# Optimization experiments

Measured on AMD Instinct MI355X. Metric: run time of the kernel, lower is better.

## Reference

```python
import jax, jax.numpy as jnp
import numpy as np

PS = 2      # patch_size
TOPK = 3    # topk


def setup_inputs() -> dict:
    key = jax.random.key(0)
    x = jax.random.normal(key, (16, 128, 64, 64), dtype=jnp.float32)
    alpha = jnp.asarray(5.0, dtype=jnp.float32)
    return {"x": x, "alpha": alpha}


def reference(x, alpha):
    ps = PS
    b, c, h, w = x.shape
    nph, npw = h // ps, w // ps
    npatch = nph * npw
    pa = ps * ps
    # F.normalize(x, p=2, dim=-3): L2-normalize over channels
    nrm = jnp.sqrt(jnp.sum(x * x, axis=1, keepdims=True))
    x = x / jnp.maximum(nrm, 1e-12)
    # patchify: [b,c,h,w] -> [b,c,num_patches,patch_area]
    x = x.reshape(b * c * nph, ps, npw, ps)
    x = jnp.swapaxes(x, 1, 2).reshape(b, c, npatch, pa)
    diag = np.arange(ps) * (ps + 1)          # diagonal positions within a patch
    x = x[:, :, :, diag]                     # [b,c,npatch,ps]
    x = jnp.swapaxes(x, 1, 3)                # [b,ps,npatch,c]
    # per-diagonal-pixel patch correlation matrix
    corr = jnp.einsum('bpnc,bpmc->bpnm', x, x)           # [b,ps,np,np]
    avg = jnp.mean(corr, axis=1, keepdims=True)
    corr = jnp.concatenate([corr, avg], axis=1)          # [b,ps+1,np,np]
    # gaussian self-suppression mask (1 - gaussian centered at each patch)
    rat_s = 0.05
    sr, sc = nph * rat_s, npw * rat_s
    ind_r = jnp.arange(nph, dtype=jnp.float32).reshape(1, nph, 1)
    ind_c = jnp.arange(npw, dtype=jnp.float32).reshape(1, 1, npw)
    cr, cc = jnp.meshgrid(jnp.arange(nph, dtype=jnp.float32),
                          jnp.arange(npw, dtype=jnp.float32), indexing='ij')
    cent_r = cr.reshape(npatch, 1, 1)
    cent_c = cc.reshape(npatch, 1, 1)
    g = jnp.exp(-(ind_r - cent_r) ** 2 / (2.0 * sr * sr)) \
        * jnp.exp(-(ind_c - cent_c) ** 2 / (2.0 * sc * sc))   # [np,nph,npw]
    mask = (1.0 - g).reshape(1, 1, npatch, npatch)
    s = (corr * mask) * alpha
    # dual (row + column) softmax
    a = jax.nn.softmax(s, axis=-1) * jax.nn.softmax(s, axis=-2)  # [b,ps+1,np,np]
    # scatter: diagonal in-patch pixels get their own map, rest get the avg map
    src = np.full(pa, ps, dtype=np.int64)
    src[diag] = np.arange(ps)
    a = a[:, src]                              # [b,pa,np,np]
    # un-patchify attention back to [b, npatch, h, w]
    a = jnp.swapaxes(a, 1, 3)                  # [b,np,np,pa]
    a = a.reshape(b * npatch * nph, npw, ps, ps)
    a = jnp.swapaxes(a, 1, 2)
    a = a.reshape(b, npatch, h, w)
    # top-k over the patch (correlation-source) dim
    vals = jax.lax.top_k(jnp.moveaxis(a, 1, -1), TOPK)[0]  # [b,h,w,k]
    return jnp.moveaxis(vals, -1, 1)           # [b,k,h,w]
```

## Files before the change

### kernel.cpp

```cpp
#include <hip/hip_runtime.h>
#include <math.h>

#define NB 16
#define NCH 128
#define NH 64
#define NW 64
#define NP 1024

#define TN 32
#define TM 128
#define KC 32
#define KP 36
#define PK 40

#define NTILE 144

typedef __attribute__((ext_vector_type(8))) short short8v;
typedef __attribute__((ext_vector_type(4))) float f32x4;

__device__ __forceinline__ float med3(float a, float b, float c) {
  return __builtin_amdgcn_fmed3f(a, b, c);
}
__device__ __forceinline__ void top3_ins(float& t0, float& t1, float& t2, float a) {
  float n0 = fmaxf(t0, a);
  float n1 = med3(a, t0, t1);
  float n2 = med3(a, t1, t2);
  t0 = n0; t1 = n1; t2 = n2;
}
__device__ __forceinline__ float dot4(float4 a, float4 b) {
  return a.x * b.x + a.y * b.y + a.z * b.z + a.w * b.w;
}
__device__ __forceinline__ ushort f2bf(float f) {
  unsigned u = __float_as_uint(f);
  unsigned r = (u + 0x7FFFu + ((u >> 16) & 1u)) >> 16;
  return (ushort)r;
}
__device__ __forceinline__ float bf2f(ushort h) {
  return __uint_as_float(((unsigned)h) << 16);
}

__global__ __launch_bounds__(256) void prep_split(const float* __restrict__ x,
                                                  ushort* __restrict__ Vs,
                                                  float* __restrict__ rsum) {
  int blk = blockIdx.x;
  int t = threadIdx.x;
  int gid = blk * 256 + t;
  if (gid < NB * 3 * NP) rsum[gid] = 0.f;

  int b = blk >> 5;
  int c = (blk >> 4) & 1;
  int ng = blk & 15;
  int nl = t >> 2;
  int kq = t & 3;
  int n = ng * 64 + nl;
  int i = 2 * (n >> 5) + c;
  int j = 2 * (n & 31) + c;
  const float* xp = x + (size_t)b * NCH * NH * NW + i * NW + j;

  float v[32];
#pragma unroll
  for (int e = 0; e < 32; ++e)
    v[e] = xp[(size_t)(kq * 32 + e) * NH * NW];

  float ss = 0.f;
#pragma unroll
  for (int e = 0; e < 32; ++e) ss += v[e] * v[e];
  ss += __shfl_xor(ss, 1, 64);
  ss += __shfl_xor(ss, 2, 64);
  float r = 1.0f / fmaxf(sqrtf(ss), 1e-12f);

  size_t base = ((size_t)(b * 2 + c) * 3) * NP * NCH + (size_t)n * NCH + kq * 32;
  ushort* p1 = Vs + base;
  ushort* p2 = Vs + base + (size_t)NP * NCH;
  ushort* p3 = Vs + base + (size_t)2 * NP * NCH;
#pragma unroll
  for (int kg2 = 0; kg2 < 4; ++kg2) {
    ushort h1[8], h2[8], h3[8];
#pragma unroll
    for (int e = 0; e < 8; ++e) {
      float vv = v[kg2 * 8 + e] * r;
      ushort a = f2bf(vv);
      float r1 = vv - bf2f(a);
      ushort bq = f2bf(r1);
      float r2 = r1 - bf2f(bq);
      ushort cq = f2bf(r2);
      h1[e] = a; h2[e] = bq; h3[e] = cq;
    }
    *(float4*)(p1 + kg2 * 8) = *(float4*)h1;
    *(float4*)(p2 + kg2 * 8) = *(float4*)h2;
    *(float4*)(p3 + kg2 * 8) = *(float4*)h3;
  }
}

__global__ __launch_bounds__(256, 2) void gemm_mfma(
    const ushort* __restrict__ Vs, const float* __restrict__ alpha_p,
    float2* __restrict__ Sbuf, float* __restrict__ rsum) {
  __shared__ __align__(16) char smem[2 * 3 * 32 * PK * 2 + 2 * 3 * 128 * PK * 2];
  ushort (*A_s)[3][32][PK] = reinterpret_cast<ushort(*)[3][32][PK]>(smem);
  ushort (*B_s)[3][128][PK] =
      reinterpret_cast<ushort(*)[3][128][PK]>(smem + 2 * 3 * 32 * PK * 2);
  float2 (*Ts)[33] = reinterpret_cast<float2(*)[33]>(smem);

  const int b = blockIdx.y;
  int id = blockIdx.x;
  int g = 0;
  while (id >= 4 * (8 - g)) { id -= 4 * (8 - g); ++g; }
  const int ni = 4 * g + id / (8 - g);
  const int mj = g + id % (8 - g);
  const int n0 = ni * TN;
  const int m0 = mj * TM;

  const int t = threadIdx.x;
  const int lane = t & 63, wv = t >> 6;
  const int jc = lane & 15, kg = lane >> 4;
  const float alpha = *alpha_p;
  const ushort* Vsb = Vs + (size_t)b * 6 * NP * NCH;
  float* rs = rsum + (size_t)b * 3 * NP;

  f32x4 acc[2][2][2];
#pragma unroll
  for (int c = 0; c < 2; ++c)
#pragma unroll
    for (int i = 0; i < 2; ++i)
#pragma unroll
      for (int j = 0; j < 2; ++j) acc[c][i][j] = (f32x4){0.f, 0.f, 0.f, 0.f};

  for (int k0 = 0; k0 < NCH; k0 += KC) {
    __syncthreads();
#pragma unroll
    for (int q = 0; q < 3; ++q) {
      int flat = q * 256 + t;
      int p = flat >> 7;
      int rem = flat & 127;
      int row = rem >> 2, u = rem & 3;
      const ushort* src = Vsb + ((size_t)p * NP + n0 + row) * NCH + k0 + u * 8;
      *(float4*)&A_s[p / 3][p % 3][row][u * 8] = *(const float4*)src;
    }
#pragma unroll
    for (int q = 0; q < 12; ++q) {
      int flat = q * 256 + t;
      int p = flat >> 9;
      int rem = flat & 511;
      int row = rem >> 2, u = rem & 3;
      const ushort* src = Vsb + ((size_t)p * NP + m0 + row) * NCH + k0 + u * 8;
      *(float4*)&B_s[p / 3][p % 3][row][u * 8] = *(const float4*)src;
    }
    __syncthreads();

#pragma unroll
    for (int c = 0; c < 2; ++c) {
      short8v a1n0 = *(const short8v*)&A_s[c][0][jc][kg * 8];
      short8v a1n1 = *(const short8v*)&A_s[c][0][16 + jc][kg * 8];
      short8v a2n0 = *(const short8v*)&A_s[c][1][jc][kg * 8];
      short8v a2n1 = *(const short8v*)&A_s[c][1][16 + jc][kg * 8];
      short8v a3n0 = *(const short8v*)&A_s[c][2][jc][kg * 8];
      short8v a3n1 = *(const short8v*)&A_s[c][2][16 + jc][kg * 8];
      {
        short8v b0 = *(const short8v*)&B_s[c][0][wv * 32 + jc][kg * 8];
        short8v b1 = *(const short8v*)&B_s[c][0][wv * 32 + 16 + jc][kg * 8];
        acc[c][0][0] = __builtin_amdgcn_mfma_f32_16x16x32_bf16(a1n0, b0, acc[c][0][0], 0, 0, 0);
        acc[c][1][0] = __builtin_amdgcn_mfma_f32_16x16x32_bf16(a1n1, b0, acc[c][1][0], 0, 0, 0);
        acc[c][0][1] = __builtin_amdgcn_mfma_f32_16x16x32_bf16(a1n0, b1, acc[c][0][1], 0, 0, 0);
        acc[c][1][1] = __builtin_amdgcn_mfma_f32_16x16x32_bf16(a1n1, b1, acc[c][1][1], 0, 0, 0);
        acc[c][0][0] = __builtin_amdgcn_mfma_f32_16x16x32_bf16(a2n0, b0, acc[c][0][0], 0, 0, 0);
        acc[c][1][0] = __builtin_amdgcn_mfma_f32_16x16x32_bf16(a2n1, b0, acc[c][1][0], 0, 0, 0);
        acc[c][0][1] = __builtin_amdgcn_mfma_f32_16x16x32_bf16(a2n0, b1, acc[c][0][1], 0, 0, 0);
        acc[c][1][1] = __builtin_amdgcn_mfma_f32_16x16x32_bf16(a2n1, b1, acc[c][1][1], 0, 0, 0);
        acc[c][0][0] = __builtin_amdgcn_mfma_f32_16x16x32_bf16(a3n0, b0, acc[c][0][0], 0, 0, 0);
        acc[c][1][0] = __builtin_amdgcn_mfma_f32_16x16x32_bf16(a3n1, b0, acc[c][1][0], 0, 0, 0);
        acc[c][0][1] = __builtin_amdgcn_mfma_f32_16x16x32_bf16(a3n0, b1, acc[c][0][1], 0, 0, 0);
        acc[c][1][1] = __builtin_amdgcn_mfma_f32_16x16x32_bf16(a3n1, b1, acc[c][1][1], 0, 0, 0);
      }
      {
        short8v b0 = *(const short8v*)&B_s[c][1][wv * 32 + jc][kg * 8];
        short8v b1 = *(const short8v*)&B_s[c][1][wv * 32 + 16 + jc][kg * 8];
        acc[c][0][0] = __builtin_amdgcn_mfma_f32_16x16x32_bf16(a1n0, b0, acc[c][0][0], 0, 0, 0);
        acc[c][1][0] = __builtin_amdgcn_mfma_f32_16x16x32_bf16(a1n1, b0, acc[c][1][0], 0, 0, 0);
        acc[c][0][1] = __builtin_amdgcn_mfma_f32_16x16x32_bf16(a1n0, b1, acc[c][0][1], 0, 0, 0);
        acc[c][1][1] = __builtin_amdgcn_mfma_f32_16x16x32_bf16(a1n1, b1, acc[c][1][1], 0, 0, 0);
        acc[c][0][0] = __builtin_amdgcn_mfma_f32_16x16x32_bf16(a2n0, b0, acc[c][0][0], 0, 0, 0);
        acc[c][1][0] = __builtin_amdgcn_mfma_f32_16x16x32_bf16(a2n1, b0, acc[c][1][0], 0, 0, 0);
        acc[c][0][1] = __builtin_amdgcn_mfma_f32_16x16x32_bf16(a2n0, b1, acc[c][0][1], 0, 0, 0);
        acc[c][1][1] = __builtin_amdgcn_mfma_f32_16x16x32_bf16(a2n1, b1, acc[c][1][1], 0, 0, 0);
      }
      {
        short8v b0 = *(const short8v*)&B_s[c][2][wv * 32 + jc][kg * 8];
        short8v b1 = *(const short8v*)&B_s[c][2][wv * 32 + 16 + jc][kg * 8];
        acc[c][0][0] = __builtin_amdgcn_mfma_f32_16x16x32_bf16(a1n0, b0, acc[c][0][0], 0, 0, 0);
        acc[c][1][0] = __builtin_amdgcn_mfma_f32_16x16x32_bf16(a1n1, b0, acc[c][1][0], 0, 0, 0);
        acc[c][0][1] = __builtin_amdgcn_mfma_f32_16x16x32_bf16(a1n0, b1, acc[c][0][1], 0, 0, 0);
        acc[c][1][1] = __builtin_amdgcn_mfma_f32_16x16x32_bf16(a1n1, b1, acc[c][1][1], 0, 0, 0);
      }
    }
  }

  __syncthreads();
  float e[2][4][3];
#pragma unroll
  for (int ns = 0; ns < 2; ++ns)
#pragma unroll
    for (int r = 0; r < 4; ++r)
#pragma unroll
      for (int c = 0; c < 3; ++c) e[ns][r][c] = 0.f;

#pragma unroll
  for (int ns = 0; ns < 2; ++ns) {
#pragma unroll
    for (int r = 0; r < 4; ++r) {
      int nl = ns * 16 + kg * 4 + r;
      int n = n0 + nl;
      int nr = n >> 5, nc = n & 31;
      float2* rowp = Sbuf + ((size_t)b * NP + n) * NP;
#pragma unroll
      for (int ms = 0; ms < 2; ++ms) {
        int ml = wv * 32 + ms * 16 + jc;
        int m = m0 + ml;
        int dr = nr - (m >> 5);
        int dc = nc - (m & 31);
        float gss = __expf(-(float)(dr * dr + dc * dc) * 0.1953125f);
        float wgt = (1.0f - gss) * alpha;
        float2 sv = make_float2(acc[0][ns][ms][r] * wgt, acc[1][ns][ms][r] * wgt);
        Ts[ml][nl] = sv;
        if (m >= n) {
          rowp[m] = sv;
          e[ns][r][0] += __expf(sv.x);
          e[ns][r][1] += __expf(sv.y);
          e[ns][r][2] += __expf(0.5f * (sv.x + sv.y));
        }
      }
    }
  }
#pragma unroll
  for (int off = 1; off < 16; off <<= 1) {
#pragma unroll
    for (int ns = 0; ns < 2; ++ns)
#pragma unroll
      for (int r = 0; r < 4; ++r)
#pragma unroll
        for (int c = 0; c < 3; ++c)
          e[ns][r][c] += __shfl_xor(e[ns][r][c], off, 64);
  }
  if (jc == 0) {
#pragma unroll
    for (int ns = 0; ns < 2; ++ns)
#pragma unroll
      for (int r = 0; r < 4; ++r)
#pragma unroll
        for (int c = 0; c < 3; ++c)
          atomicAdd(&rs[(size_t)c * NP + (n0 + ns * 16 + kg * 4 + r)], e[ns][r][c]);
  }

  __syncthreads();
#pragma unroll
  for (int q = 0; q < 16; ++q) {
    int flat = q * 256 + t;
    int ml = flat >> 5;
    int r = flat & 31;
    int m = m0 + ml;
    int n = n0 + r;
    if (m > n) Sbuf[((size_t)b * NP + m) * NP + n] = Ts[ml][r];
  }
  {
    int ml = t >> 1;
    int rh = (t & 1) * 16;
    int m = m0 + ml;
    float e0 = 0.f, e1 = 0.f, e2 = 0.f;
#pragma unroll
    for (int rr = 0; rr < 16; ++rr) {
      int r = rh + rr;
      int n = n0 + r;
      float2 sv = Ts[ml][r];
      if (m > n) {
        e0 += __expf(sv.x);
        e1 += __expf(sv.y);
        e2 += __expf(0.5f * (sv.x + sv.y));
      }
    }
    e0 += __shfl_xor(e0, 1, 64);
    e1 += __shfl_xor(e1, 1, 64);
    e2 += __shfl_xor(e2, 1, 64);
    if ((t & 1) == 0) {
      atomicAdd(&rs[(size_t)0 * NP + m], e0);
      atomicAdd(&rs[(size_t)1 * NP + m], e1);
      atomicAdd(&rs[(size_t)2 * NP + m], e2);
    }
  }
}

__global__ __launch_bounds__(256) void recip_kernel(float* __restrict__ p, int nelem) {
  int i = blockIdx.x * 256 + threadIdx.x;
  if (i < nelem) p[i] = 1.0f / p[i];
}

__global__ __launch_bounds__(256, 4) void topk_kernel(
    const float2* __restrict__ Sbuf, const float* __restrict__ rinv,
    float* __restrict__ out) {
  const int n = blockIdx.x, b = blockIdx.y;
  const int t = threadIdx.x;
  const float* rb = rinv + (size_t)b * 3 * NP;
  float rin[3];
#pragma unroll
  for (int c = 0; c < 3; ++c) rin[c] = rb[c * NP + n];
  const float2* row = Sbuf + ((size_t)b * NP + n) * NP;

  float t0[3] = {0.f, 0.f, 0.f}, t1[3] = {0.f, 0.f, 0.f}, t2[3] = {0.f, 0.f, 0.f};
#pragma unroll
  for (int q = 0; q < 4; ++q) {
    int m = t + q * 256;
    float2 s01 = row[m];
    float s[3];
    s[0] = s01.x; s[1] = s01.y; s[2] = 0.5f * (s01.x + s01.y);
#pragma unroll
    for (int c = 0; c < 3; ++c) {
      float a = __expf(2.0f * s[c]) * rin[c] * rb[c * NP + m];
      top3_ins(t0[c], t1[c], t2[c], a);
    }
  }
#pragma unroll
  for (int off = 1; off < 64; off <<= 1) {
#pragma unroll
    for (int c = 0; c < 3; ++c) {
      float o0 = __shfl_xor(t0[c], off, 64);
      float o1 = __shfl_xor(t1[c], off, 64);
      float o2 = __shfl_xor(t2[c], off, 64);
      top3_ins(t0[c], t1[c], t2[c], o0);
      top3_ins(t0[c], t1[c], t2[c], o1);
      top3_ins(t0[c], t1[c], t2[c], o2);
    }
  }
  __shared__ float lds[4][9];
  if ((t & 63) == 0) {
    int w = t >> 6;
#pragma unroll
    for (int c = 0; c < 3; ++c) {
      lds[w][c * 3 + 0] = t0[c];
      lds[w][c * 3 + 1] = t1[c];
      lds[w][c * 3 + 2] = t2[c];
    }
  }
  __syncthreads();
  if (t == 0) {
#pragma unroll
    for (int w = 1; w < 4; ++w)
#pragma unroll
      for (int c = 0; c < 3; ++c) {
        top3_ins(t0[c], t1[c], t2[c], lds[w][c * 3 + 0]);
        top3_ins(t0[c], t1[c], t2[c], lds[w][c * 3 + 1]);
        top3_ins(t0[c], t1[c], t2[c], lds[w][c * 3 + 2]);
      }
    int pr = n >> 5, pc = n & 31;
#pragma unroll
    for (int c = 0; c < 3; ++c) {
      int ii0, jj0, ii1 = -1, jj1 = -1;
      if (c == 0)      { ii0 = 2 * pr;     jj0 = 2 * pc; }
      else if (c == 1) { ii0 = 2 * pr + 1; jj0 = 2 * pc + 1; }
      else             { ii0 = 2 * pr;     jj0 = 2 * pc + 1;
                         ii1 = 2 * pr + 1; jj1 = 2 * pc; }
      out[(((size_t)b * 3 + 0) * NH + ii0) * NW + jj0] = t0[c];
      out[(((size_t)b * 3 + 1) * NH + ii0) * NW + jj0] = t1[c];
      out[(((size_t)b * 3 + 2) * NH + ii0) * NW + jj0] = t2[c];
      if (ii1 >= 0) {
        out[(((size_t)b * 3 + 0) * NH + ii1) * NW + jj1] = t0[c];
        out[(((size_t)b * 3 + 1) * NH + ii1) * NW + jj1] = t1[c];
        out[(((size_t)b * 3 + 2) * NH + ii1) * NW + jj1] = t2[c];
      }
    }
  }
}

__global__ __launch_bounds__(256) void prep_kernel(const float* __restrict__ x,
                                                   float* __restrict__ V) {
  int blk = blockIdx.x;
  int t = threadIdx.x;
  int b = blk >> 3;
  int c = (blk >> 2) & 1;
  int n = (blk & 3) * 256 + t;
  int i = 2 * (n >> 5) + c;
  int j = 2 * (n & 31) + c;
  const float* xp = x + (size_t)b * NCH * NH * NW + i * NW + j;
  float ss = 0.f;
#pragma unroll 8
  for (int ch = 0; ch < NCH; ++ch) {
    float v = xp[(size_t)ch * NH * NW];
    ss += v * v;
  }
  float r = 1.0f / fmaxf(sqrtf(ss), 1e-12f);
  float* vp = V + (((size_t)b * 2 + c) * NP + n) * NCH;
#pragma unroll 8
  for (int ch = 0; ch < NCH; ++ch) {
    vp[ch] = xp[(size_t)ch * NH * NW] * r;
  }
}

template <int PASS>
__global__ __launch_bounds__(256, 2) void corr_kernel(
    const float* __restrict__ V, const float* __restrict__ alpha_p,
    float* __restrict__ rsum_g, float* __restrict__ out) {
  __shared__ __align__(16) float As[2][TN][KP];
  __shared__ __align__(16) float Bs[2][TM][KP];

  const int b = blockIdx.y;
  const int n0 = blockIdx.x * TN;
  const int t = threadIdx.x;
  const int tx = t & 31;
  const int ty = t >> 5;
  const float alpha = *alpha_p;
  const float* Vb = V + (size_t)b * 2 * NP * NCH;

  float sm[3][4];
  float t0[3][4], t1[3][4], t2[3][4];
  float rin[3][4];
#pragma unroll
  for (int c = 0; c < 3; ++c)
#pragma unroll
    for (int i = 0; i < 4; ++i) {
      sm[c][i] = 0.f;
      t0[c][i] = 0.f; t1[c][i] = 0.f; t2[c][i] = 0.f;
    }
  if (PASS == 2) {
#pragma unroll
    for (int c = 0; c < 3; ++c)
#pragma unroll
      for (int i = 0; i < 4; ++i) {
        int n = n0 + ty * 4 + i;
        rin[c][i] = 1.0f / rsum_g[((size_t)b * 3 + c) * NP + n];
      }
  }

  for (int mc = 0; mc < NP / TM; ++mc) {
    const int m0 = mc * TM;
    float acc[2][4][4];
#pragma unroll
    for (int c = 0; c < 2; ++c)
#pragma unroll
      for (int i = 0; i < 4; ++i)
#pragma unroll
        for (int j = 0; j < 4; ++j) acc[c][i][j] = 0.f;

    for (int k0 = 0; k0 < NCH; k0 += KC) {
      __syncthreads();
#pragma unroll
      for (int q = 0; q < 2; ++q) {
        int flat = q * 256 + t;
        int c = flat >> 8;
        int rem = flat & 255;
        int row = rem >> 3;
        int kgx = rem & 7;
        float4 v4 = *(const float4*)(Vb + ((size_t)c * NP + n0 + row) * NCH + k0 + kgx * 4);
        *(float4*)&As[c][row][kgx * 4] = v4;
      }
#pragma unroll
      for (int q = 0; q < 8; ++q) {
        int flat = q * 256 + t;
        int c = flat >> 10;
        int rem = flat & 1023;
        int row = rem >> 3;
        int kgx = rem & 7;
        float4 v4 = *(const float4*)(Vb + ((size_t)c * NP + m0 + row) * NCH + k0 + kgx * 4);
        *(float4*)&Bs[c][row][kgx * 4] = v4;
      }
      __syncthreads();

      for (int kgx = 0; kgx < KC; kgx += 4) {
        float4 a4[2][4], b4[2][4];
#pragma unroll
        for (int c = 0; c < 2; ++c)
#pragma unroll
          for (int i = 0; i < 4; ++i)
            a4[c][i] = *(const float4*)&As[c][ty * 4 + i][kgx];
#pragma unroll
        for (int c = 0; c < 2; ++c)
#pragma unroll
          for (int j = 0; j < 4; ++j)
            b4[c][j] = *(const float4*)&Bs[c][tx + 32 * j][kgx];
#pragma unroll
        for (int c = 0; c < 2; ++c)
#pragma unroll
          for (int i = 0; i < 4; ++i)
#pragma unroll
            for (int j = 0; j < 4; ++j)
              acc[c][i][j] += dot4(a4[c][i], b4[c][j]);
      }
    }

    float rim[3][4];
    if (PASS == 2) {
#pragma unroll
      for (int c = 0; c < 3; ++c)
#pragma unroll
        for (int j = 0; j < 4; ++j) {
          int m = m0 + tx + 32 * j;
          rim[c][j] = 1.0f / rsum_g[((size_t)b * 3 + c) * NP + m];
        }
    }
#pragma unroll
    for (int i = 0; i < 4; ++i) {
      int n = n0 + ty * 4 + i;
      int nr = n >> 5, nc = n & 31;
      float s[3][4];
#pragma unroll
      for (int j = 0; j < 4; ++j) {
        int m = m0 + tx + 32 * j;
        int dr = nr - (m >> 5);
        int dc = nc - (m & 31);
        float gq = __expf(-(float)(dr * dr + dc * dc) * 0.1953125f);
        float wgt = (1.0f - gq) * alpha;
        float s0v = acc[0][i][j] * wgt;
        float s1v = acc[1][i][j] * wgt;
        s[0][j] = s0v; s[1][j] = s1v; s[2][j] = 0.5f * (s0v + s1v);
      }
      if (PASS == 1) {
#pragma unroll
        for (int c = 0; c < 3; ++c) {
          sm[c][i] += __expf(s[c][0]) + __expf(s[c][1]) +
                      __expf(s[c][2]) + __expf(s[c][3]);
        }
      } else {
#pragma unroll
        for (int c = 0; c < 3; ++c) {
#pragma unroll
          for (int j = 0; j < 4; ++j) {
            float a = __expf(2.0f * s[c][j]) * rin[c][i] * rim[c][j];
            top3_ins(t0[c][i], t1[c][i], t2[c][i], a);
          }
        }
      }
    }
  }

  if (PASS == 1) {
#pragma unroll
    for (int off = 1; off < 32; off <<= 1) {
#pragma unroll
      for (int c = 0; c < 3; ++c)
#pragma unroll
        for (int i = 0; i < 4; ++i)
          sm[c][i] += __shfl_xor(sm[c][i], off, 64);
    }
    if (tx == 0) {
#pragma unroll
      for (int c = 0; c < 3; ++c)
#pragma unroll
        for (int i = 0; i < 4; ++i) {
          int n = n0 + ty * 4 + i;
          rsum_g[((size_t)b * 3 + c) * NP + n] = sm[c][i];
        }
    }
  } else {
#pragma unroll
    for (int off = 1; off < 32; off <<= 1) {
#pragma unroll
      for (int c = 0; c < 3; ++c)
#pragma unroll
        for (int i = 0; i < 4; ++i) {
          float o0 = __shfl_xor(t0[c][i], off, 64);
          float o1 = __shfl_xor(t1[c][i], off, 64);
          float o2 = __shfl_xor(t2[c][i], off, 64);
          top3_ins(t0[c][i], t1[c][i], t2[c][i], o0);
          top3_ins(t0[c][i], t1[c][i], t2[c][i], o1);
          top3_ins(t0[c][i], t1[c][i], t2[c][i], o2);
        }
    }
    if (tx == 0) {
#pragma unroll
      for (int c = 0; c < 3; ++c)
#pragma unroll
        for (int i = 0; i < 4; ++i) {
          int n = n0 + ty * 4 + i;
          int pr = n >> 5, pc = n & 31;
          float v0 = t0[c][i], v1 = t1[c][i], v2 = t2[c][i];
          int ii0, jj0, ii1 = -1, jj1 = -1;
          if (c == 0)      { ii0 = 2 * pr;     jj0 = 2 * pc; }
          else if (c == 1) { ii0 = 2 * pr + 1; jj0 = 2 * pc + 1; }
          else             { ii0 = 2 * pr;     jj0 = 2 * pc + 1;
                             ii1 = 2 * pr + 1; jj1 = 2 * pc; }
          out[(((size_t)b * 3 + 0) * NH + ii0) * NW + jj0] = v0;
          out[(((size_t)b * 3 + 1) * NH + ii0) * NW + jj0] = v1;
          out[(((size_t)b * 3 + 2) * NH + ii0) * NW + jj0] = v2;
          if (ii1 >= 0) {
            out[(((size_t)b * 3 + 0) * NH + ii1) * NW + jj1] = v0;
            out[(((size_t)b * 3 + 1) * NH + ii1) * NW + jj1] = v1;
            out[(((size_t)b * 3 + 2) * NH + ii1) * NW + jj1] = v2;
          }
        }
    }
  }
}

extern "C" void kernel_launch(void* const* d_in, const int* in_sizes, int n_in,
                              void* d_out, int out_size, void* d_ws, size_t ws_size,
                              hipStream_t stream) {
  const float* x = (const float*)d_in[0];
  const float* alpha = (const float*)d_in[1];
  float* out = (float*)d_out;

  const size_t nVsU = (size_t)NB * 6 * NP * NCH;
  const size_t nRs = (size_t)NB * 3 * NP;
  const size_t nS = (size_t)NB * NP * NP;

  ushort* Vs = (ushort*)d_ws;
  float* rsum = (float*)(Vs + nVsU);
  float2* Sbuf = (float2*)(rsum + nRs);

  const size_t need_bytes = nVsU * 2 + nRs * 4 + nS * 8;

  if (ws_size >= need_bytes) {
    prep_split<<<512, 256, 0, stream>>>(x, Vs, rsum);
    gemm_mfma<<<dim3(NTILE, NB), 256, 0, stream>>>(Vs, alpha, Sbuf, rsum);
    recip_kernel<<<(NB * 3 * NP + 255) / 256, 256, 0, stream>>>(rsum, NB * 3 * NP);
    topk_kernel<<<dim3(NP, NB), 256, 0, stream>>>(Sbuf, rsum, out);
  } else {
    float* V = (float*)d_ws;
    float* rsum_f = V + (size_t)NB * 2 * NP * NCH;
    prep_kernel<<<128, 256, 0, stream>>>(x, V);
    corr_kernel<1><<<dim3(NP / TN, NB), 256, 0, stream>>>(V, alpha, rsum_f, out);
    corr_kernel<2><<<dim3(NP / TN, NB), 256, 0, stream>>>(V, alpha, rsum_f, out);
  }
}
```

Measured before the change: 148.6 us.

## Recompute correlation tiles in top-k kernel instead of materializing score matrix

The full 1024x1024 score matrix per batch is no longer written to and read back from global memory. The first GEMM pass now only accumulates softmax row and column exp-sums, with the transposed column sums reduced in registers through shuffles instead of an LDS transpose. A new MFMA top-k kernel recomputes the split-bf16 correlation for a 16-row strip against all columns and applies the dual-softmax and top-3 selection on the fly. This removes a large HBM round trip in exchange for recomputing the full, non-symmetric GEMM and re-reading the B operand from cache once per 16-row strip.

```diff
diff --git a/kernel.cpp b/kernel.cpp
--- a/kernel.cpp
+++ b/kernel.cpp
@@ -92,14 +92,13 @@
   }
 }
 
-__global__ __launch_bounds__(256, 2) void gemm_mfma(
+__global__ __launch_bounds__(256, 2) void rowsum_mfma(
     const ushort* __restrict__ Vs, const float* __restrict__ alpha_p,
-    float2* __restrict__ Sbuf, float* __restrict__ rsum) {
+    float* __restrict__ rsum) {
   __shared__ __align__(16) char smem[2 * 3 * 32 * PK * 2 + 2 * 3 * 128 * PK * 2];
   ushort (*A_s)[3][32][PK] = reinterpret_cast<ushort(*)[3][32][PK]>(smem);
   ushort (*B_s)[3][128][PK] =
       reinterpret_cast<ushort(*)[3][128][PK]>(smem + 2 * 3 * 32 * PK * 2);
-  float2 (*Ts)[33] = reinterpret_cast<float2(*)[33]>(smem);
 
   const int b = blockIdx.y;
   int id = blockIdx.x;
@@ -194,39 +193,40 @@
     }
   }
 
-  __syncthreads();
   float e[2][4][3];
+  float gcol[2][3];
 #pragma unroll
   for (int ns = 0; ns < 2; ++ns)
 #pragma unroll
     for (int r = 0; r < 4; ++r)
 #pragma unroll
       for (int c = 0; c < 3; ++c) e[ns][r][c] = 0.f;
-
+#pragma unroll
+  for (int ms = 0; ms < 2; ++ms)
+#pragma unroll
+    for (int c = 0; c < 3; ++c) gcol[ms][c] = 0.f;
+
+  const float alpha_l = alpha;
 #pragma unroll
   for (int ns = 0; ns < 2; ++ns) {
 #pragma unroll
     for (int r = 0; r < 4; ++r) {
-      int nl = ns * 16 + kg * 4 + r;
-      int n = n0 + nl;
+      int n = n0 + ns * 16 + kg * 4 + r;
       int nr = n >> 5, nc = n & 31;
-      float2* rowp = Sbuf + ((size_t)b * NP + n) * NP;
 #pragma unroll
       for (int ms = 0; ms < 2; ++ms) {
-        int ml = wv * 32 + ms * 16 + jc;
-        int m = m0 + ml;
+        int m = m0 + wv * 32 + ms * 16 + jc;
         int dr = nr - (m >> 5);
         int dc = nc - (m & 31);
         float gss = __expf(-(float)(dr * dr + dc * dc) * 0.1953125f);
-        float wgt = (1.0f - gss) * alpha;
-        float2 sv = make_float2(acc[0][ns][ms][r] * wgt, acc[1][ns][ms][r] * wgt);
-        Ts[ml][nl] = sv;
-        if (m >= n) {
-          rowp[m] = sv;
-          e[ns][r][0] += __expf(sv.x);
-          e[ns][r][1] += __expf(sv.y);
-          e[ns][r][2] += __expf(0.5f * (sv.x + sv.y));
-        }
+        float wgt = (1.0f - gss) * alpha_l;
+        float s0 = acc[0][ns][ms][r] * wgt;
+        float s1 = acc[1][ns][ms][r] * wgt;
+        float e0 = __expf(s0);
+        float e1 = __expf(s1);
+        float e2 = __expf(0.5f * (s0 + s1));
+        if (m >= n) { e[ns][r][0] += e0; e[ns][r][1] += e1; e[ns][r][2] += e2; }
+        if (m > n)  { gcol[ms][0] += e0; gcol[ms][1] += e1; gcol[ms][2] += e2; }
       }
     }
   }
@@ -249,40 +249,21 @@
         for (int c = 0; c < 3; ++c)
           atomicAdd(&rs[(size_t)c * NP + (n0 + ns * 16 + kg * 4 + r)], e[ns][r][c]);
   }
-
-  __syncthreads();
-#pragma unroll
-  for (int q = 0; q < 16; ++q) {
-    int flat = q * 256 + t;
-    int ml = flat >> 5;
-    int r = flat & 31;
-    int m = m0 + ml;
-    int n = n0 + r;
-    if (m > n) Sbuf[((size_t)b * NP + m) * NP + n] = Ts[ml][r];
-  }
-  {
-    int ml = t >> 1;
-    int rh = (t & 1) * 16;
-    int m = m0 + ml;
-    float e0 = 0.f, e1 = 0.f, e2 = 0.f;
-#pragma unroll
-    for (int rr = 0; rr < 16; ++rr) {
-      int r = rh + rr;
-      int n = n0 + r;
-      float2 sv = Ts[ml][r];
-      if (m > n) {
-        e0 += __expf(sv.x);
-        e1 += __expf(sv.y);
-        e2 += __expf(0.5f * (sv.x + sv.y));
-      }
-    }
-    e0 += __shfl_xor(e0, 1, 64);
-    e1 += __shfl_xor(e1, 1, 64);
-    e2 += __shfl_xor(e2, 1, 64);
-    if ((t & 1) == 0) {
-      atomicAdd(&rs[(size_t)0 * NP + m], e0);
-      atomicAdd(&rs[(size_t)1 * NP + m], e1);
-      atomicAdd(&rs[(size_t)2 * NP + m], e2);
+#pragma unroll
+  for (int off = 16; off < 64; off <<= 1) {
+#pragma unroll
+    for (int ms = 0; ms < 2; ++ms)
+#pragma unroll
+      for (int c = 0; c < 3; ++c)
+        gcol[ms][c] += __shfl_xor(gcol[ms][c], off, 64);
+  }
+  if (kg == 0) {
+#pragma unroll
+    for (int ms = 0; ms < 2; ++ms) {
+      int m = m0 + wv * 32 + ms * 16 + jc;
+#pragma unroll
+      for (int c = 0; c < 3; ++c)
+        atomicAdd(&rs[(size_t)c * NP + m], gcol[ms][c]);
     }
   }
 }
@@ -292,78 +273,179 @@
   if (i < nelem) p[i] = 1.0f / p[i];
 }
 
-__global__ __launch_bounds__(256, 4) void topk_kernel(
-    const float2* __restrict__ Sbuf, const float* __restrict__ rinv,
-    float* __restrict__ out) {
-  const int n = blockIdx.x, b = blockIdx.y;
+__global__ __launch_bounds__(256, 2) void topk_mfma(
+    const ushort* __restrict__ Vs, const float* __restrict__ alpha_p,
+    const float* __restrict__ rinv, float* __restrict__ out) {
+  __shared__ __align__(16) char smem[2 * 3 * 16 * PK * 2 + 2 * 3 * 128 * PK * 2];
+  ushort (*A_s)[3][16][PK] = reinterpret_cast<ushort(*)[3][16][PK]>(smem);
+  ushort (*B_s)[3][128][PK] =
+      reinterpret_cast<ushort(*)[3][128][PK]>(smem + 2 * 3 * 16 * PK * 2);
+
+  const int b = blockIdx.y;
+  const int n0 = blockIdx.x * 16;
   const int t = threadIdx.x;
-  const float* rb = rinv + (size_t)b * 3 * NP;
-  float rin[3];
-#pragma unroll
-  for (int c = 0; c < 3; ++c) rin[c] = rb[c * NP + n];
-  const float2* row = Sbuf + ((size_t)b * NP + n) * NP;
-
-  float t0[3] = {0.f, 0.f, 0.f}, t1[3] = {0.f, 0.f, 0.f}, t2[3] = {0.f, 0.f, 0.f};
-#pragma unroll
-  for (int q = 0; q < 4; ++q) {
-    int m = t + q * 256;
-    float2 s01 = row[m];
-    float s[3];
-    s[0] = s01.x; s[1] = s01.y; s[2] = 0.5f * (s01.x + s01.y);
-#pragma unroll
-    for (int c = 0; c < 3; ++c) {
-      float a = __expf(2.0f * s[c]) * rin[c] * rb[c * NP + m];
-      top3_ins(t0[c], t1[c], t2[c], a);
-    }
-  }
-#pragma unroll
-  for (int off = 1; off < 64; off <<= 1) {
-#pragma unroll
-    for (int c = 0; c < 3; ++c) {
-      float o0 = __shfl_xor(t0[c], off, 64);
-      float o1 = __shfl_xor(t1[c], off, 64);
-      float o2 = __shfl_xor(t2[c], off, 64);
-      top3_ins(t0[c], t1[c], t2[c], o0);
-      top3_ins(t0[c], t1[c], t2[c], o1);
-      top3_ins(t0[c], t1[c], t2[c], o2);
-    }
-  }
-  __shared__ float lds[4][9];
-  if ((t & 63) == 0) {
-    int w = t >> 6;
-#pragma unroll
-    for (int c = 0; c < 3; ++c) {
-      lds[w][c * 3 + 0] = t0[c];
-      lds[w][c * 3 + 1] = t1[c];
-      lds[w][c * 3 + 2] = t2[c];
-    }
-  }
+  const int lane = t & 63, wv = t >> 6;
+  const int jc = lane & 15, kg = lane >> 4;
+  const float alpha = *alpha_p;
+  const ushort* Vsb = Vs + (size_t)b * 6 * NP * NCH;
+  const float* rs = rinv + (size_t)b * 3 * NP;
+
+  float rin[3][4];
+#pragma unroll
+  for (int c = 0; c < 3; ++c)
+#pragma unroll
+    for (int r = 0; r < 4; ++r)
+      rin[c][r] = rs[(size_t)c * NP + (n0 + kg * 4 + r)];
+
+  float t0[3][4], t1[3][4], t2[3][4];
+#pragma unroll
+  for (int c = 0; c < 3; ++c)
+#pragma unroll
+    for (int r = 0; r < 4; ++r) { t0[c][r] = 0.f; t1[c][r] = 0.f; t2[c][r] = 0.f; }
+
+  for (int mc = 0; mc < 8; ++mc) {
+    const int m0 = mc * TM;
+    f32x4 acc[2][2];
+#pragma unroll
+    for (int c = 0; c < 2; ++c)
+#pragma unroll
+      for (int j = 0; j < 2; ++j) acc[c][j] = (f32x4){0.f, 0.f, 0.f, 0.f};
+
+    for (int k0 = 0; k0 < NCH; k0 += KC) {
+      __syncthreads();
+#pragma unroll
+      for (int q = 0; q < 2; ++q) {
+        int flat = q * 256 + t;
+        if (flat < 384) {
+          int p = flat >> 6;
+          int rem = flat & 63;
+          int row = rem >> 2, u = rem & 3;
+          const ushort* src = Vsb + ((size_t)p * NP + n0 + row) * NCH + k0 + u * 8;
+          *(float4*)&A_s[p / 3][p % 3][row][u * 8] = *(const float4*)src;
+        }
+      }
+#pragma unroll
+      for (int q = 0; q < 12; ++q) {
+        int flat = q * 256 + t;
+        int p = flat >> 9;
+        int rem = flat & 511;
+        int row = rem >> 2, u = rem & 3;
+        const ushort* src = Vsb + ((size_t)p * NP + m0 + row) * NCH + k0 + u * 8;
+        *(float4*)&B_s[p / 3][p % 3][row][u * 8] = *(const float4*)src;
+      }
+      __syncthreads();
+
+#pragma unroll
+      for (int c = 0; c < 2; ++c) {
+        short8v a1 = *(const short8v*)&A_s[c][0][jc][kg * 8];
+        short8v a2 = *(const short8v*)&A_s[c][1][jc][kg * 8];
+        short8v a3 = *(const short8v*)&A_s[c][2][jc][kg * 8];
+        {
+          short8v b0 = *(const short8v*)&B_s[c][0][wv * 32 + jc][kg * 8];
+          short8v b1 = *(const short8v*)&B_s[c][0][wv * 32 + 16 + jc][kg * 8];
+          acc[c][0] = __builtin_amdgcn_mfma_f32_16x16x32_bf16(a1, b0, acc[c][0], 0, 0, 0);
+          acc[c][1] = __builtin_amdgcn_mfma_f32_16x16x32_bf16(a1, b1, acc[c][1], 0, 0, 0);
+          acc[c][0] = __builtin_amdgcn_mfma_f32_16x16x32_bf16(a2, b0, acc[c][0], 0, 0, 0);
+          acc[c][1] = __builtin_amdgcn_mfma_f32_16x16x32_bf16(a2, b1, acc[c][1], 0, 0, 0);
+          acc[c][0] = __builtin_amdgcn_mfma_f32_16x16x32_bf16(a3, b0, acc[c][0], 0, 0, 0);
+          acc[c][1] = __builtin_amdgcn_mfma_f32_16x16x32_bf16(a3, b1, acc[c][1], 0, 0, 0);
+        }
+        {
+          short8v b0 = *(const short8v*)&B_s[c][1][wv * 32 + jc][kg * 8];
+          short8v b1 = *(const short8v*)&B_s[c][1][wv * 32 + 16 + jc][kg * 8];
+          acc[c][0] = __builtin_amdgcn_mfma_f32_16x16x32_bf16(a1, b0, acc[c][0], 0, 0, 0);
+          acc[c][1] = __builtin_amdgcn_mfma_f32_16x16x32_bf16(a1, b1, acc[c][1], 0, 0, 0);
+          acc[c][0] = __builtin_amdgcn_mfma_f32_16x16x32_bf16(a2, b0, acc[c][0], 0, 0, 0);
+          acc[c][1] = __builtin_amdgcn_mfma_f32_16x16x32_bf16(a2, b1, acc[c][1], 0, 0, 0);
+        }
+        {
+          short8v b0 = *(const short8v*)&B_s[c][2][wv * 32 + jc][kg * 8];
+          short8v b1 = *(const short8v*)&B_s[c][2][wv * 32 + 16 + jc][kg * 8];
+          acc[c][0] = __builtin_amdgcn_mfma_f32_16x16x32_bf16(a1, b0, acc[c][0], 0, 0, 0);
+          acc[c][1] = __builtin_amdgcn_mfma_f32_16x16x32_bf16(a1, b1, acc[c][1], 0, 0, 0);
+        }
+      }
+    }
+
+#pragma unroll
+    for (int ms = 0; ms < 2; ++ms) {
+      int m = m0 + wv * 32 + ms * 16 + jc;
+      float rim0 = rs[(size_t)0 * NP + m];
+      float rim1 = rs[(size_t)1 * NP + m];
+      float rim2 = rs[(size_t)2 * NP + m];
+      int mr = m >> 5, mcw = m & 31;
+#pragma unroll
+      for (int r = 0; r < 4; ++r) {
+        int n = n0 + kg * 4 + r;
+        int dr = (n >> 5) - mr;
+        int dc = (n & 31) - mcw;
+        float gss = __expf(-(float)(dr * dr + dc * dc) * 0.1953125f);
+        float wgt = (1.0f - gss) * alpha;
+        float s0 = acc[0][ms][r] * wgt;
+        float s1 = acc[1][ms][r] * wgt;
+        float a0 = __expf(2.0f * s0) * rin[0][r] * rim0;
+        float a1 = __expf(2.0f * s1) * rin[1][r] * rim1;
+        float a2 = __expf(s0 + s1) * rin[2][r] * rim2;
+        top3_ins(t0[0][r], t1[0][r], t2[0][r], a0);
+        top3_ins(t0[1][r], t1[1][r], t2[1][r], a1);
+        top3_ins(t0[2][r], t1[2][r], t2[2][r], a2);
+      }
+    }
+  }
+
+#pragma unroll
+  for (int off = 1; off < 16; off <<= 1) {
+#pragma unroll
+    for (int c = 0; c < 3; ++c)
+#pragma unroll
+      for (int r = 0; r < 4; ++r) {
+        float o0 = __shfl_xor(t0[c][r], off, 64);
+        float o1 = __shfl_xor(t1[c][r], off, 64);
+        float o2 = __shfl_xor(t2[c][r], off, 64);
+        top3_ins(t0[c][r], t1[c][r], t2[c][r], o0);
+        top3_ins(t0[c][r], t1[c][r], t2[c][r], o1);
+        top3_ins(t0[c][r], t1[c][r], t2[c][r], o2);
+      }
+  }
+
   __syncthreads();
-  if (t == 0) {
-#pragma unroll
-    for (int w = 1; w < 4; ++w)
+  float* mb = (float*)smem;
+  if (jc == 0) {
+#pragma unroll
+    for (int r = 0; r < 4; ++r) {
+      int row = kg * 4 + r;
 #pragma unroll
       for (int c = 0; c < 3; ++c) {
-        top3_ins(t0[c], t1[c], t2[c], lds[w][c * 3 + 0]);
-        top3_ins(t0[c], t1[c], t2[c], lds[w][c * 3 + 1]);
-        top3_ins(t0[c], t1[c], t2[c], lds[w][c * 3 + 2]);
-      }
+        mb[((wv * 16) + row) * 9 + c * 3 + 0] = t0[c][r];
+        mb[((wv * 16) + row) * 9 + c * 3 + 1] = t1[c][r];
+        mb[((wv * 16) + row) * 9 + c * 3 + 2] = t2[c][r];
+      }
+    }
+  }
+  __syncthreads();
+  if (t < 48) {
+    int row = t / 3, c = t % 3;
+    float u0 = 0.f, u1 = 0.f, u2 = 0.f;
+#pragma unroll
+    for (int w = 0; w < 4; ++w) {
+      top3_ins(u0, u1, u2, mb[(w * 16 + row) * 9 + c * 3 + 0]);
+      top3_ins(u0, u1, u2, mb[(w * 16 + row) * 9 + c * 3 + 1]);
+      top3_ins(u0, u1, u2, mb[(w * 16 + row) * 9 + c * 3 + 2]);
+    }
+    int n = n0 + row;
     int pr = n >> 5, pc = n & 31;
-#pragma unroll
-    for (int c = 0; c < 3; ++c) {
-      int ii0, jj0, ii1 = -1, jj1 = -1;
-      if (c == 0)      { ii0 = 2 * pr;     jj0 = 2 * pc; }
-      else if (c == 1) { ii0 = 2 * pr + 1; jj0 = 2 * pc + 1; }
-      else             { ii0 = 2 * pr;     jj0 = 2 * pc + 1;
-                         ii1 = 2 * pr + 1; jj1 = 2 * pc; }
-      out[(((size_t)b * 3 + 0) * NH + ii0) * NW + jj0] = t0[c];
-      out[(((size_t)b * 3 + 1) * NH + ii0) * NW + jj0] = t1[c];
-      out[(((size_t)b * 3 + 2) * NH + ii0) * NW + jj0] = t2[c];
-      if (ii1 >= 0) {
-        out[(((size_t)b * 3 + 0) * NH + ii1) * NW + jj1] = t0[c];
-        out[(((size_t)b * 3 + 1) * NH + ii1) * NW + jj1] = t1[c];
-        out[(((size_t)b * 3 + 2) * NH + ii1) * NW + jj1] = t2[c];
-      }
+    int ii0, jj0, ii1 = -1, jj1 = -1;
+    if (c == 0)      { ii0 = 2 * pr;     jj0 = 2 * pc; }
+    else if (c == 1) { ii0 = 2 * pr + 1; jj0 = 2 * pc + 1; }
+    else             { ii0 = 2 * pr;     jj0 = 2 * pc + 1;
+                       ii1 = 2 * pr + 1; jj1 = 2 * pc; }
+    out[(((size_t)b * 3 + 0) * NH + ii0) * NW + jj0] = u0;
+    out[(((size_t)b * 3 + 1) * NH + ii0) * NW + jj0] = u1;
+    out[(((size_t)b * 3 + 2) * NH + ii0) * NW + jj0] = u2;
+    if (ii1 >= 0) {
+      out[(((size_t)b * 3 + 0) * NH + ii1) * NW + jj1] = u0;
+      out[(((size_t)b * 3 + 1) * NH + ii1) * NW + jj1] = u1;
+      out[(((size_t)b * 3 + 2) * NH + ii1) * NW + jj1] = u2;
     }
   }
 }
@@ -596,19 +678,17 @@
 
   const size_t nVsU = (size_t)NB * 6 * NP * NCH;
   const size_t nRs = (size_t)NB * 3 * NP;
-  const size_t nS = (size_t)NB * NP * NP;
 
   ushort* Vs = (ushort*)d_ws;
   float* rsum = (float*)(Vs + nVsU);
-  float2* Sbuf = (float2*)(rsum + nRs);
-
-  const size_t need_bytes = nVsU * 2 + nRs * 4 + nS * 8;
+
+  const size_t need_bytes = nVsU * 2 + nRs * 4;
 
   if (ws_size >= need_bytes) {
     prep_split<<<512, 256, 0, stream>>>(x, Vs, rsum);
-    gemm_mfma<<<dim3(NTILE, NB), 256, 0, stream>>>(Vs, alpha, Sbuf, rsum);
+    rowsum_mfma<<<dim3(NTILE, NB), 256, 0, stream>>>(Vs, alpha, rsum);
     recip_kernel<<<(NB * 3 * NP + 255) / 256, 256, 0, stream>>>(rsum, NB * 3 * NP);
-    topk_kernel<<<dim3(NP, NB), 256, 0, stream>>>(Sbuf, rsum, out);
+    topk_mfma<<<dim3(NP / 16, NB), 256, 0, stream>>>(Vs, alpha, rsum, out);
   } else {
     float* V = (float*)d_ws;
     float* rsum_f = V + (size_t)NB * 2 * NP * NCH;
```

Result: slower. 229.2 us (+54.2%).
